# Kernel optimization log

Measured on AMD Instinct MI355X. Metric: run time of the kernel, lower is better.

The kernel has to match this reference:

```python
import jax, jax.numpy as jnp
import numpy as np

NEG_INF = -jnp.inf

def setup_inputs() -> dict:
    key = jax.random.key(0)
    k1, k2, k3, k4, k5 = jax.random.split(key, 5)
    b, n, d = 8, 1024, 2048
    s = 1.0 / np.sqrt(d)  # keep activations well-scaled (kaiming-ish)
    return {
        "y":  jax.random.normal(k1, (b, n, d), dtype=jnp.float32),
        "Wk": jax.random.normal(k2, (d, d), dtype=jnp.float32) * s,
        "Wq": jax.random.normal(k3, (d, d), dtype=jnp.float32) * s,
        "Wv": jax.random.normal(k4, (d, d), dtype=jnp.float32) * s,
        "Wo": jax.random.normal(k5, (d, d), dtype=jnp.float32) * s,
    }

def reference(y, Wk, Wq, Wv, Wo):
    # nn.Linear(bias=False): x @ W.T
    K = jnp.einsum('bnd,ed->bne', y, Wk)
    Q = 0.1 * jnp.einsum('bnd,ed->bne', y, Wq)
    V = jnp.einsum('bnd,ed->bne', y, Wv)
    # logits[b,i,j] = Q_i . K_j
    logits = jnp.einsum('bid,bjd->bij', Q, K)
    n = y.shape[1]
    diag = jnp.eye(n, dtype=bool)  # self-exclusion mask on the diagonal
    logits = jnp.where(diag[None, :, :], NEG_INF, logits)
    # NOTE: softmax over dim=1 (rows of the score matrix), non-standard axis
    attention_weights = jax.nn.softmax(logits, axis=1)
    # dropout(p=0.5) treated as identity (eval/deterministic reference)
    # torch: (V^T @ W)^T  ==  out[b,i,:] = sum_j W[b,j,i] * V[b,j,:]
    out = jnp.einsum('bji,bjd->bid', attention_weights, V)
    out = jnp.einsum('bid,ed->bie', out, Wo)
    return (out, attention_weights)
```

## Files before the change

### kernel.cpp

```cpp
#include <hip/hip_runtime.h>

typedef unsigned short u16;
typedef __attribute__((ext_vector_type(8))) __bf16 bf16x8;
typedef __attribute__((ext_vector_type(4))) float f32x4;
typedef __attribute__((ext_vector_type(4))) unsigned short u16x4;
typedef __attribute__((ext_vector_type(8))) unsigned short u16x8;

#define GLOBAL_AS __attribute__((address_space(1)))
#define LDS_AS __attribute__((address_space(3)))

__device__ __forceinline__ void gload_lds16(const void* g, void* l) {
    __builtin_amdgcn_global_load_lds((const GLOBAL_AS void*)g, (LDS_AS void*)l, 16, 0, 0);
}

__device__ __forceinline__ u16 f2bf(float f) {
    union { float f; unsigned u; } x; x.f = f;
    unsigned r = x.u + 0x7FFFu + ((x.u >> 16) & 1u);
    return (u16)(r >> 16);
}
__device__ __forceinline__ float bf2f(u16 h) {
    union { unsigned u; float f; } x; x.u = ((unsigned)h) << 16;
    return x.f;
}
struct BfPair { u16 h, l; };
__device__ __forceinline__ BfPair split2(float v) {
    BfPair p;
    p.h = f2bf(v);
    p.l = f2bf(v - bf2f(p.h));
    return p;
}

#define TM 128
#define TN 128
#define BK 64

__global__ __launch_bounds__(256) void conv_bf(
    const float* __restrict__ src, u16* __restrict__ dst, int n8)
{
    const int stride = gridDim.x * 256;
    for (int i = blockIdx.x * 256 + threadIdx.x; i < n8; i += stride) {
        const float* g = src + (size_t)i * 8;
        f32x4 v0 = *(const f32x4*)g;
        f32x4 v1 = *(const f32x4*)(g + 4);
        u16x8 w;
        #pragma unroll
        for (int e = 0; e < 4; ++e) { w[e] = f2bf(v0[e]); w[e + 4] = f2bf(v1[e]); }
        *(u16x8*)(dst + (size_t)i * 8) = w;
    }
}

__global__ __launch_bounds__(256) void transpose3(
    const float* __restrict__ s0, const float* __restrict__ s1, const float* __restrict__ s2,
    u16* __restrict__ d0, u16* __restrict__ d1, u16* __restrict__ d2)
{
    __shared__ float tile[64][65];
    const int z = blockIdx.z;
    const float* S = (z == 0) ? s0 : (z == 1) ? s1 : s2;
    u16* D = (z == 0) ? d0 : (z == 1) ? d1 : d2;
    const int x0 = blockIdx.x * 64;
    const int y0 = blockIdx.y * 64;
    const int t = threadIdx.x;
    const int rt = t >> 4;
    const int c4 = (t & 15) * 4;

    #pragma unroll
    for (int p = 0; p < 4; ++p) {
        const int r = p * 16 + rt;
        f32x4 v = *(const f32x4*)(S + (size_t)(y0 + r) * 2048 + x0 + c4);
        #pragma unroll
        for (int e = 0; e < 4; ++e) tile[r][c4 + e] = v[e];
    }
    __syncthreads();
    #pragma unroll
    for (int p = 0; p < 4; ++p) {
        const int a = p * 16 + rt;
        u16x4 w;
        #pragma unroll
        for (int e = 0; e < 4; ++e) w[e] = f2bf(tile[c4 + e][a]);
        *(u16x4*)(D + (size_t)(x0 + a) * 2048 + y0 + c4) = w;
    }
}

__global__ __launch_bounds__(256) void gemm_pre2(
    const u16* __restrict__ A0, const u16* __restrict__ B0,
    u16* __restrict__ GH, u16* __restrict__ GL, float alpha0,
    const u16* __restrict__ A1, const u16* __restrict__ B1, u16* __restrict__ U1,
    int M, int N, int K)
{
    __shared__ u16 As[TM * BK];
    __shared__ u16 Bs[TN * BK];

    const int z = blockIdx.z;
    const u16* Ab = z ? A1 : A0;
    const u16* Bb = z ? B1 : B0;

    const int n0 = blockIdx.x * TN;
    const int m0 = blockIdx.y * TM;
    const int tid = threadIdx.x;
    const int lane = tid & 63;
    const int wave = tid >> 6;
    const int wm = (wave >> 1) * 64;
    const int wn = (wave & 1) * 64;
    const int quad = lane >> 4;
    const int lrow = lane & 15;

    f32x4 acc[4][4] = {};

    for (int k0 = 0; k0 < K; k0 += BK) {
        #pragma unroll
        for (int r = 0; r < 4; ++r) {
            const int wbase = r * 4096 + wave * 1024;
            const int o = wbase + lane * 16;
            const int row = o >> 7;
            const int ce = (o & 127) >> 1;
            gload_lds16(Ab + (size_t)(m0 + row) * K + k0 + ce, (char*)As + wbase);
            gload_lds16(Bb + (size_t)(n0 + row) * K + k0 + ce, (char*)Bs + wbase);
        }
        __syncthreads();

        #pragma unroll
        for (int kk = 0; kk < BK; kk += 32) {
            bf16x8 af[4], bfr[4];
            #pragma unroll
            for (int t = 0; t < 4; ++t) {
                af[t]  = *(const bf16x8*)&As[(wm + t * 16 + lrow) * BK + kk + quad * 8];
                bfr[t] = *(const bf16x8*)&Bs[(wn + t * 16 + lrow) * BK + kk + quad * 8];
            }
            #pragma unroll
            for (int ti = 0; ti < 4; ++ti)
                #pragma unroll
                for (int tj = 0; tj < 4; ++tj)
                    acc[ti][tj] = __builtin_amdgcn_mfma_f32_16x16x32_bf16(
                        af[ti], bfr[tj], acc[ti][tj], 0, 0, 0);
        }
        __syncthreads();
    }

    #pragma unroll
    for (int ti = 0; ti < 4; ++ti)
        #pragma unroll
        for (int tj = 0; tj < 4; ++tj) {
            const int nn = n0 + wn + tj * 16 + lrow;
            #pragma unroll
            for (int r2 = 0; r2 < 4; ++r2) {
                const int mm = m0 + wm + ti * 16 + quad * 4 + r2;
                if (z == 0) {
                    BfPair p = split2(acc[ti][tj][r2] * alpha0);
                    GH[(size_t)mm * N + nn] = p.h;
                    GL[(size_t)mm * N + nn] = p.l;
                } else {
                    U1[(size_t)mm * N + nn] = f2bf(acc[ti][tj][r2]);
                }
            }
        }
}

template <bool OSPLIT>
__global__ __launch_bounds__(256) void gemm_bf(
    const u16* __restrict__ A, const u16* __restrict__ B,
    u16* __restrict__ Ch, u16* __restrict__ Cl,
    int M, int N, int K, size_t sAb, size_t sBb, size_t sCb, float alpha)
{
    __shared__ u16 As[TM * BK];
    __shared__ u16 Bs[TN * BK];

    const int z = blockIdx.z;
    const u16* Ab = (const u16*)((const char*)A + (size_t)z * sAb);
    const u16* Bb = (const u16*)((const char*)B + (size_t)z * sBb);

    const int n0 = blockIdx.x * TN;
    const int m0 = blockIdx.y * TM;
    const int tid = threadIdx.x;
    const int lane = tid & 63;
    const int wave = tid >> 6;
    const int wm = (wave >> 1) * 64;
    const int wn = (wave & 1) * 64;
    const int quad = lane >> 4;
    const int lrow = lane & 15;

    f32x4 acc[4][4] = {};

    for (int k0 = 0; k0 < K; k0 += BK) {
        #pragma unroll
        for (int r = 0; r < 4; ++r) {
            const int wbase = r * 4096 + wave * 1024;
            const int o = wbase + lane * 16;
            const int row = o >> 7;
            const int ce = (o & 127) >> 1;
            gload_lds16(Ab + (size_t)(m0 + row) * K + k0 + ce, (char*)As + wbase);
            gload_lds16(Bb + (size_t)(n0 + row) * K + k0 + ce, (char*)Bs + wbase);
        }
        __syncthreads();

        #pragma unroll
        for (int kk = 0; kk < BK; kk += 32) {
            bf16x8 af[4], bfr[4];
            #pragma unroll
            for (int t = 0; t < 4; ++t) {
                af[t]  = *(const bf16x8*)&As[(wm + t * 16 + lrow) * BK + kk + quad * 8];
                bfr[t] = *(const bf16x8*)&Bs[(wn + t * 16 + lrow) * BK + kk + quad * 8];
            }
            #pragma unroll
            for (int ti = 0; ti < 4; ++ti)
                #pragma unroll
                for (int tj = 0; tj < 4; ++tj)
                    acc[ti][tj] = __builtin_amdgcn_mfma_f32_16x16x32_bf16(
                        af[ti], bfr[tj], acc[ti][tj], 0, 0, 0);
        }
        __syncthreads();
    }

    u16* Chb = (u16*)((char*)Ch + (size_t)z * sCb);
    u16* Clb = OSPLIT ? (u16*)((char*)Cl + (size_t)z * sCb) : nullptr;
    #pragma unroll
    for (int ti = 0; ti < 4; ++ti)
        #pragma unroll
        for (int tj = 0; tj < 4; ++tj) {
            const int nn = n0 + wn + tj * 16 + lrow;
            #pragma unroll
            for (int r2 = 0; r2 < 4; ++r2) {
                const int mm = m0 + wm + ti * 16 + quad * 4 + r2;
                if (OSPLIT) {
                    BfPair p = split2(acc[ti][tj][r2] * alpha);
                    Chb[(size_t)mm * N + nn] = p.h;
                    Clb[(size_t)mm * N + nn] = p.l;
                } else {
                    Chb[(size_t)mm * N + nn] = f2bf(acc[ti][tj][r2] * alpha);
                }
            }
        }
}

template <bool OSPLIT>
__global__ __launch_bounds__(256) void gemm_bs(
    const u16* __restrict__ A,
    const u16* __restrict__ Bh, const u16* __restrict__ Bl,
    void* __restrict__ C, void* __restrict__ C2,
    int M, int N, int K, size_t sAb, size_t sBb, size_t sCb)
{
    __shared__ u16 As[TM * BK];
    __shared__ u16 Bsh[TN * BK];
    __shared__ u16 Bsl[TN * BK];

    const int z = blockIdx.z;
    const u16* Ab  = (const u16*)((const char*)A + (size_t)z * sAb);
    const u16* Bhb = (const u16*)((const char*)Bh + (size_t)z * sBb);
    const u16* Blb = (const u16*)((const char*)Bl + (size_t)z * sBb);

    const int n0 = blockIdx.x * TN;
    const int m0 = blockIdx.y * TM;
    const int tid = threadIdx.x;
    const int lane = tid & 63;
    const int wave = tid >> 6;
    const int wm = (wave >> 1) * 64;
    const int wn = (wave & 1) * 64;
    const int quad = lane >> 4;
    const int lrow = lane & 15;

    f32x4 acc[4][4] = {};

    for (int k0 = 0; k0 < K; k0 += BK) {
        #pragma unroll
        for (int r = 0; r < 4; ++r) {
            const int wbase = r * 4096 + wave * 1024;
            const int o = wbase + lane * 16;
            const int row = o >> 7;
            const int ce = (o & 127) >> 1;
            const size_t ao = (size_t)(m0 + row) * K + k0 + ce;
            const size_t bo = (size_t)(n0 + row) * K + k0 + ce;
            gload_lds16(Ab + ao, (char*)As + wbase);
            gload_lds16(Bhb + bo, (char*)Bsh + wbase);
            gload_lds16(Blb + bo, (char*)Bsl + wbase);
        }
        __syncthreads();

        #pragma unroll
        for (int kk = 0; kk < BK; kk += 32) {
            bf16x8 af[4], bh[4], bl[4];
            #pragma unroll
            for (int t = 0; t < 4; ++t) {
                const int ra = (wm + t * 16 + lrow) * BK + kk + quad * 8;
                const int rb = (wn + t * 16 + lrow) * BK + kk + quad * 8;
                af[t] = *(const bf16x8*)&As[ra];
                bh[t] = *(const bf16x8*)&Bsh[rb];
                bl[t] = *(const bf16x8*)&Bsl[rb];
            }
            #pragma unroll
            for (int ti = 0; ti < 4; ++ti)
                #pragma unroll
                for (int tj = 0; tj < 4; ++tj) {
                    acc[ti][tj] = __builtin_amdgcn_mfma_f32_16x16x32_bf16(
                        af[ti], bl[tj], acc[ti][tj], 0, 0, 0);
                    acc[ti][tj] = __builtin_amdgcn_mfma_f32_16x16x32_bf16(
                        af[ti], bh[tj], acc[ti][tj], 0, 0, 0);
                }
        }
        __syncthreads();
    }

    if (OSPLIT) {
        u16* Chb = (u16*)((char*)C + (size_t)z * sCb);
        u16* Clb = (u16*)((char*)C2 + (size_t)z * sCb);
        #pragma unroll
        for (int ti = 0; ti < 4; ++ti)
            #pragma unroll
            for (int tj = 0; tj < 4; ++tj) {
                const int nn = n0 + wn + tj * 16 + lrow;
                #pragma unroll
                for (int r2 = 0; r2 < 4; ++r2) {
                    const int mm = m0 + wm + ti * 16 + quad * 4 + r2;
                    BfPair p = split2(acc[ti][tj][r2]);
                    Chb[(size_t)mm * N + nn] = p.h;
                    Clb[(size_t)mm * N + nn] = p.l;
                }
            }
    } else {
        float* Cb = (float*)((char*)C + (size_t)z * sCb);
        #pragma unroll
        for (int ti = 0; ti < 4; ++ti)
            #pragma unroll
            for (int tj = 0; tj < 4; ++tj) {
                const int nn = n0 + wn + tj * 16 + lrow;
                #pragma unroll
                for (int r2 = 0; r2 < 4; ++r2) {
                    const int mm = m0 + wm + ti * 16 + quad * 4 + r2;
                    Cb[(size_t)mm * N + nn] = acc[ti][tj][r2];
                }
            }
    }
}

__global__ __launch_bounds__(256) void gemm_fin(
    const u16* __restrict__ Ah, const u16* __restrict__ Al,
    const u16* __restrict__ B, float* __restrict__ C,
    int M, int N, int K, size_t sAb, size_t sBb, size_t sCb)
{
    __shared__ u16 Ash[TM * BK];
    __shared__ u16 Asl[TM * BK];
    __shared__ u16 Bs[TN * BK];

    const int z = blockIdx.z;
    const u16* Ahb = (const u16*)((const char*)Ah + (size_t)z * sAb);
    const u16* Alb = (const u16*)((const char*)Al + (size_t)z * sAb);
    const u16* Bb  = (const u16*)((const char*)B + (size_t)z * sBb);

    const int n0 = blockIdx.x * TN;
    const int m0 = blockIdx.y * TM;
    const int tid = threadIdx.x;
    const int lane = tid & 63;
    const int wave = tid >> 6;
    const int wm = (wave >> 1) * 64;
    const int wn = (wave & 1) * 64;
    const int quad = lane >> 4;
    const int lrow = lane & 15;

    f32x4 acc[4][4] = {};

    for (int k0 = 0; k0 < K; k0 += BK) {
        #pragma unroll
        for (int r = 0; r < 4; ++r) {
            const int wbase = r * 4096 + wave * 1024;
            const int o = wbase + lane * 16;
            const int row = o >> 7;
            const int ce = (o & 127) >> 1;
            const size_t ao = (size_t)(m0 + row) * K + k0 + ce;
            const size_t bo = (size_t)(n0 + row) * K + k0 + ce;
            gload_lds16(Ahb + ao, (char*)Ash + wbase);
            gload_lds16(Alb + ao, (char*)Asl + wbase);
            gload_lds16(Bb + bo, (char*)Bs + wbase);
        }
        __syncthreads();

        #pragma unroll
        for (int kk = 0; kk < BK; kk += 32) {
            bf16x8 ah[4], al[4], bfr[4];
            #pragma unroll
            for (int t = 0; t < 4; ++t) {
                const int ra = (wm + t * 16 + lrow) * BK + kk + quad * 8;
                ah[t] = *(const bf16x8*)&Ash[ra];
                al[t] = *(const bf16x8*)&Asl[ra];
                bfr[t] = *(const bf16x8*)&Bs[(wn + t * 16 + lrow) * BK + kk + quad * 8];
            }
            #pragma unroll
            for (int ti = 0; ti < 4; ++ti)
                #pragma unroll
                for (int tj = 0; tj < 4; ++tj) {
                    acc[ti][tj] = __builtin_amdgcn_mfma_f32_16x16x32_bf16(
                        al[ti], bfr[tj], acc[ti][tj], 0, 0, 0);
                    acc[ti][tj] = __builtin_amdgcn_mfma_f32_16x16x32_bf16(
                        ah[ti], bfr[tj], acc[ti][tj], 0, 0, 0);
                }
        }
        __syncthreads();
    }

    float* Cb = (float*)((char*)C + (size_t)z * sCb);
    #pragma unroll
    for (int ti = 0; ti < 4; ++ti)
        #pragma unroll
        for (int tj = 0; tj < 4; ++tj) {
            const int nn = n0 + wn + tj * 16 + lrow;
            #pragma unroll
            for (int r2 = 0; r2 < 4; ++r2) {
                const int mm = m0 + wm + ti * 16 + quad * 4 + r2;
                Cb[(size_t)mm * N + nn] = acc[ti][tj][r2];
            }
        }
}

__global__ __launch_bounds__(256) void softmax_split(
    const float* __restrict__ Lh, u16* __restrict__ Th, u16* __restrict__ Tl)
{
    const int lane = threadIdx.x & 63;
    const int wave = threadIdx.x >> 6;
    const size_t row = (size_t)blockIdx.x * 4 + wave;
    const int i = (int)(row & 1023);
    const float* src = Lh + row * 1024;
    const float NEG = -__builtin_inff();

    float v[16];
    float mx = NEG;
    #pragma unroll
    for (int cc = 0; cc < 4; ++cc) {
        f32x4 x = *(const f32x4*)(src + cc * 256 + lane * 4);
        #pragma unroll
        for (int e = 0; e < 4; ++e) {
            const int j = cc * 256 + lane * 4 + e;
            const float val = (j == i) ? NEG : x[e];
            v[cc * 4 + e] = val;
            mx = fmaxf(mx, val);
        }
    }
    #pragma unroll
    for (int off = 32; off > 0; off >>= 1) mx = fmaxf(mx, __shfl_xor(mx, off, 64));
    float s = 0.f;
    #pragma unroll
    for (int k = 0; k < 16; ++k) { v[k] = __expf(v[k] - mx); s += v[k]; }
    #pragma unroll
    for (int off = 32; off > 0; off >>= 1) s += __shfl_xor(s, off, 64);
    const float inv = 1.0f / s;

    #pragma unroll
    for (int cc = 0; cc < 4; ++cc) {
        u16x4 wh, wl;
        #pragma unroll
        for (int e = 0; e < 4; ++e) {
            BfPair p = split2(v[cc * 4 + e] * inv);
            wh[e] = p.h;
            wl[e] = p.l;
        }
        *(u16x4*)(Th + row * 1024 + cc * 256 + lane * 4) = wh;
        *(u16x4*)(Tl + row * 1024 + cc * 256 + lane * 4) = wl;
    }
}

__global__ __launch_bounds__(256) void transpose_attn_f32(
    const u16* __restrict__ Th, const u16* __restrict__ Tl, float* __restrict__ A)
{
    __shared__ float tile[64][65];
    const int bz = blockIdx.z;
    const int x0 = blockIdx.x * 64;
    const int y0 = blockIdx.y * 64;
    const size_t base = (size_t)bz * 1024 * 1024;
    float* dst = A + base;
    const int t = threadIdx.x;
    const int rt = t >> 4;
    const int c4 = (t & 15) * 4;

    #pragma unroll
    for (int p = 0; p < 4; ++p) {
        const int r = p * 16 + rt;
        const size_t off = base + (size_t)(y0 + r) * 1024 + x0 + c4;
        u16x4 vh = *(const u16x4*)(Th + off);
        u16x4 vl = *(const u16x4*)(Tl + off);
        #pragma unroll
        for (int e = 0; e < 4; ++e) tile[r][c4 + e] = bf2f(vh[e]) + bf2f(vl[e]);
    }
    __syncthreads();
    #pragma unroll
    for (int p = 0; p < 4; ++p) {
        const int a = p * 16 + rt;
        f32x4 w;
        #pragma unroll
        for (int e = 0; e < 4; ++e) w[e] = tile[c4 + e][a];
        *(f32x4*)(dst + (size_t)(x0 + a) * 1024 + y0 + c4) = w;
    }
}

extern "C" void kernel_launch(void* const* d_in, const int* in_sizes, int n_in,
                              void* d_out, int out_size, void* d_ws, size_t ws_size,
                              hipStream_t stream) {
    const float* y  = (const float*)d_in[0];
    const float* Wk = (const float*)d_in[1];
    const float* Wq = (const float*)d_in[2];
    const float* Wv = (const float*)d_in[3];
    const float* Wo = (const float*)d_in[4];

    const int b = 8, n = 1024, d = 2048;
    const int MB = b * n;
    const size_t MiB = 1024 * 1024;

    char* ws = (char*)d_ws;
    u16* yB  = (u16*)(ws);
    u16* WkT = (u16*)(ws + 32 * MiB);
    u16* WqT = (u16*)(ws + 40 * MiB);
    u16* WvT = (u16*)(ws + 48 * MiB);
    u16* WoB = (u16*)(ws + 56 * MiB);
    u16* GtH = (u16*)(ws + 64 * MiB);
    u16* GtL = (u16*)(ws + 72 * MiB);
    u16* UtB = (u16*)(ws + 80 * MiB);
    u16* ZcH = (u16*)(ws + 32 * MiB);
    u16* ZcL = (u16*)(ws + 88 * MiB);
    u16* Th  = (u16*)(ws + 32 * MiB);
    u16* Tl  = (u16*)(ws + 48 * MiB);
    u16* VOt = (u16*)(ws + 88 * MiB);

    float* outF = (float*)d_out;
    float* attF = outF + (size_t)MB * d;
    float* Lh   = (float*)d_out;

    dim3 blk(256);
    conv_bf<<<dim3(2048), blk, 0, stream>>>(y,  yB,  (MB * d) / 8);
    conv_bf<<<dim3(512),  blk, 0, stream>>>(Wo, WoB, (d * d) / 8);
    transpose3<<<dim3(32, 32, 3), blk, 0, stream>>>(Wk, Wq, Wv, WkT, WqT, WvT);
    gemm_pre2<<<dim3(d / TN, d / TM, 2), blk, 0, stream>>>(
        WkT, WqT, GtH, GtL, 0.1f, WoB, WvT, UtB, d, d, d);
    gemm_bs<true><<<dim3(d / TN, MB / TM, 1), blk, 0, stream>>>(
        yB, GtH, GtL, ZcH, ZcL, MB, d, d, 0, 0, 0);
    gemm_bs<false><<<dim3(n / TN, n / TM, b), blk, 0, stream>>>(
        yB, ZcH, ZcL, Lh, nullptr, n, n, d,
        (size_t)n * d * 2, (size_t)n * d * 2, (size_t)n * n * 4);
    softmax_split<<<dim3(MB / 4), blk, 0, stream>>>(Lh, Th, Tl);
    transpose_attn_f32<<<dim3(16, 16, b), blk, 0, stream>>>(Th, Tl, attF);
    gemm_bf<false><<<dim3(n / TN, d / TM, b), blk, 0, stream>>>(
        UtB, yB, VOt, nullptr, d, n, d, 0, (size_t)n * d * 2, (size_t)d * n * 2, 1.0f);
    gemm_fin<<<dim3(d / TN, n / TM, b), blk, 0, stream>>>(
        Th, Tl, VOt, outF, n, d, n,
        (size_t)n * n * 2, (size_t)d * n * 2, (size_t)n * d * 4);
}
```

Baseline: 656.8 us.

## Replace final two GEMMs with triple-buffered swizzled 256x128 pipelined GEMM kernel

Adds a gemm_dp kernel with 512 threads, a 256x128 output tile, a three-stage LDS ring filled via global_load_lds, and an XOR-swizzled LDS layout. A partial vmcnt wait lets the next tiles load while the current one is being computed. The final hi/lo split product becomes a single GEMM over a concatenated K axis (Th then Tl against VOt twice), replacing the paired MFMAs per step. The aim is to hide memory latency and reduce LDS bank conflicts. The cost is about 147KB of LDS per block, so only one block fits per CU despite the launch bound of two.

Measured after the change: 677.1 us. 3.1% more time.

```diff
diff --git a/kernel.cpp b/kernel.cpp
--- a/kernel.cpp
+++ b/kernel.cpp
@@ -150,82 +150,6 @@
                     GL[(size_t)mm * N + nn] = p.l;
                 } else {
                     U1[(size_t)mm * N + nn] = f2bf(acc[ti][tj][r2]);
-                }
-            }
-        }
-}
-
-template <bool OSPLIT>
-__global__ __launch_bounds__(256) void gemm_bf(
-    const u16* __restrict__ A, const u16* __restrict__ B,
-    u16* __restrict__ Ch, u16* __restrict__ Cl,
-    int M, int N, int K, size_t sAb, size_t sBb, size_t sCb, float alpha)
-{
-    __shared__ u16 As[TM * BK];
-    __shared__ u16 Bs[TN * BK];
-
-    const int z = blockIdx.z;
-    const u16* Ab = (const u16*)((const char*)A + (size_t)z * sAb);
-    const u16* Bb = (const u16*)((const char*)B + (size_t)z * sBb);
-
-    const int n0 = blockIdx.x * TN;
-    const int m0 = blockIdx.y * TM;
-    const int tid = threadIdx.x;
-    const int lane = tid & 63;
-    const int wave = tid >> 6;
-    const int wm = (wave >> 1) * 64;
-    const int wn = (wave & 1) * 64;
-    const int quad = lane >> 4;
-    const int lrow = lane & 15;
-
-    f32x4 acc[4][4] = {};
-
-    for (int k0 = 0; k0 < K; k0 += BK) {
-        #pragma unroll
-        for (int r = 0; r < 4; ++r) {
-            const int wbase = r * 4096 + wave * 1024;
-            const int o = wbase + lane * 16;
-            const int row = o >> 7;
-            const int ce = (o & 127) >> 1;
-            gload_lds16(Ab + (size_t)(m0 + row) * K + k0 + ce, (char*)As + wbase);
-            gload_lds16(Bb + (size_t)(n0 + row) * K + k0 + ce, (char*)Bs + wbase);
-        }
-        __syncthreads();
-
-        #pragma unroll
-        for (int kk = 0; kk < BK; kk += 32) {
-            bf16x8 af[4], bfr[4];
-            #pragma unroll
-            for (int t = 0; t < 4; ++t) {
-                af[t]  = *(const bf16x8*)&As[(wm + t * 16 + lrow) * BK + kk + quad * 8];
-                bfr[t] = *(const bf16x8*)&Bs[(wn + t * 16 + lrow) * BK + kk + quad * 8];
-            }
-            #pragma unroll
-            for (int ti = 0; ti < 4; ++ti)
-                #pragma unroll
-                for (int tj = 0; tj < 4; ++tj)
-                    acc[ti][tj] = __builtin_amdgcn_mfma_f32_16x16x32_bf16(
-                        af[ti], bfr[tj], acc[ti][tj], 0, 0, 0);
-        }
-        __syncthreads();
-    }
-
-    u16* Chb = (u16*)((char*)Ch + (size_t)z * sCb);
-    u16* Clb = OSPLIT ? (u16*)((char*)Cl + (size_t)z * sCb) : nullptr;
-    #pragma unroll
-    for (int ti = 0; ti < 4; ++ti)
-        #pragma unroll
-        for (int tj = 0; tj < 4; ++tj) {
-            const int nn = n0 + wn + tj * 16 + lrow;
-            #pragma unroll
-            for (int r2 = 0; r2 < 4; ++r2) {
-                const int mm = m0 + wm + ti * 16 + quad * 4 + r2;
-                if (OSPLIT) {
-                    BfPair p = split2(acc[ti][tj][r2] * alpha);
-                    Chb[(size_t)mm * N + nn] = p.h;
-                    Clb[(size_t)mm * N + nn] = p.l;
-                } else {
-                    Chb[(size_t)mm * N + nn] = f2bf(acc[ti][tj][r2] * alpha);
                 }
             }
         }
@@ -330,80 +254,120 @@
     }
 }
 
-__global__ __launch_bounds__(256) void gemm_fin(
-    const u16* __restrict__ Ah, const u16* __restrict__ Al,
-    const u16* __restrict__ B, float* __restrict__ C,
-    int M, int N, int K, size_t sAb, size_t sBb, size_t sCb)
-{
-    __shared__ u16 Ash[TM * BK];
-    __shared__ u16 Asl[TM * BK];
-    __shared__ u16 Bs[TN * BK];
+#define DBM 256
+#define DBN 128
+template <int EPI>
+__global__ __launch_bounds__(512, 2) void gemm_dp(
+    const u16* __restrict__ A0, const u16* __restrict__ A1, int halfKA, int ldA, size_t sAb,
+    const u16* __restrict__ B0, const u16* __restrict__ B1, int halfKB, int ldB, size_t sBb,
+    void* __restrict__ C, size_t sCb, int M, int N, int Ktot)
+{
+    __shared__ alignas(16) u16 As[3 * DBM * BK];
+    __shared__ alignas(16) u16 Bs[3 * DBN * BK];
 
     const int z = blockIdx.z;
-    const u16* Ahb = (const u16*)((const char*)Ah + (size_t)z * sAb);
-    const u16* Alb = (const u16*)((const char*)Al + (size_t)z * sAb);
-    const u16* Bb  = (const u16*)((const char*)B + (size_t)z * sBb);
-
-    const int n0 = blockIdx.x * TN;
-    const int m0 = blockIdx.y * TM;
+    const u16* A0b = (const u16*)((const char*)A0 + (size_t)z * sAb);
+    const u16* A1b = (const u16*)((const char*)A1 + (size_t)z * sAb);
+    const u16* B0b = (const u16*)((const char*)B0 + (size_t)z * sBb);
+    const u16* B1b = (const u16*)((const char*)B1 + (size_t)z * sBb);
+
+    const int n0 = blockIdx.x * DBN;
+    const int m0 = blockIdx.y * DBM;
     const int tid = threadIdx.x;
     const int lane = tid & 63;
-    const int wave = tid >> 6;
-    const int wm = (wave >> 1) * 64;
-    const int wn = (wave & 1) * 64;
+    const int wid = tid >> 6;
+    const int wr = wid >> 1;
+    const int wc = wid & 1;
     const int quad = lane >> 4;
     const int lrow = lane & 15;
 
+    int arow[4], acol[4], brow[2], bcol[2];
+    #pragma unroll
+    for (int s = 0; s < 4; ++s) {
+        const int o = s * 8192 + tid * 16;
+        const int L = o ^ (((o >> 9) & 1) << 5);
+        arow[s] = L >> 7; acol[s] = L & 127;
+    }
+    #pragma unroll
+    for (int s = 0; s < 2; ++s) {
+        const int o = s * 8192 + tid * 16;
+        const int L = o ^ (((o >> 9) & 1) << 5);
+        brow[s] = L >> 7; bcol[s] = L & 127;
+    }
+    const int ldst = wid * 1024;
+
+    const int NT = Ktot / BK;
+
+    auto STAGE = [&](int tt, int bufi) {
+        const int k0 = tt * BK;
+        const u16* Ap = (k0 < halfKA) ? A0b : A1b;
+        const int ka = (k0 < halfKA) ? k0 : k0 - halfKA;
+        const u16* Bp = (k0 < halfKB) ? B0b : B1b;
+        const int kb = (k0 < halfKB) ? k0 : k0 - halfKB;
+        char* ab = (char*)As + bufi * (DBM * BK * 2);
+        char* bb = (char*)Bs + bufi * (DBN * BK * 2);
+        #pragma unroll
+        for (int s = 0; s < 4; ++s)
+            gload_lds16((const char*)Ap + ((size_t)(m0 + arow[s]) * ldA + ka) * 2 + acol[s],
+                        ab + s * 8192 + ldst);
+        #pragma unroll
+        for (int s = 0; s < 2; ++s)
+            gload_lds16((const char*)Bp + ((size_t)(n0 + brow[s]) * ldB + kb) * 2 + bcol[s],
+                        bb + s * 8192 + ldst);
+    };
+
     f32x4 acc[4][4] = {};
 
-    for (int k0 = 0; k0 < K; k0 += BK) {
-        #pragma unroll
-        for (int r = 0; r < 4; ++r) {
-            const int wbase = r * 4096 + wave * 1024;
-            const int o = wbase + lane * 16;
-            const int row = o >> 7;
-            const int ce = (o & 127) >> 1;
-            const size_t ao = (size_t)(m0 + row) * K + k0 + ce;
-            const size_t bo = (size_t)(n0 + row) * K + k0 + ce;
-            gload_lds16(Ahb + ao, (char*)Ash + wbase);
-            gload_lds16(Alb + ao, (char*)Asl + wbase);
-            gload_lds16(Bb + bo, (char*)Bs + wbase);
-        }
-        __syncthreads();
-
+    STAGE(0, 0); STAGE(1, 1); STAGE(2, 2);
+
+    int cur = 0;
+    for (int t = 0; t < NT; ++t) {
+        asm volatile("s_waitcnt vmcnt(12)" ::: "memory");
+        __builtin_amdgcn_s_barrier();
+        __builtin_amdgcn_sched_barrier(0);
+
+        const char* ab = (const char*)As + cur * (DBM * BK * 2);
+        const char* bb = (const char*)Bs + cur * (DBN * BK * 2);
         #pragma unroll
         for (int kk = 0; kk < BK; kk += 32) {
-            bf16x8 ah[4], al[4], bfr[4];
-            #pragma unroll
-            for (int t = 0; t < 4; ++t) {
-                const int ra = (wm + t * 16 + lrow) * BK + kk + quad * 8;
-                ah[t] = *(const bf16x8*)&Ash[ra];
-                al[t] = *(const bf16x8*)&Asl[ra];
-                bfr[t] = *(const bf16x8*)&Bs[(wn + t * 16 + lrow) * BK + kk + quad * 8];
+            bf16x8 af[4], bfr[4];
+            const int cbase = kk * 2 + quad * 16;
+            #pragma unroll
+            for (int f = 0; f < 4; ++f) {
+                const int ra = wr * 64 + f * 16 + lrow;
+                af[f] = *(const bf16x8*)(ab + ra * 128 + (cbase ^ (((ra >> 2) & 1) << 5)));
+                const int rb = wc * 64 + f * 16 + lrow;
+                bfr[f] = *(const bf16x8*)(bb + rb * 128 + (cbase ^ (((rb >> 2) & 1) << 5)));
             }
             #pragma unroll
             for (int ti = 0; ti < 4; ++ti)
                 #pragma unroll
-                for (int tj = 0; tj < 4; ++tj) {
+                for (int tj = 0; tj < 4; ++tj)
                     acc[ti][tj] = __builtin_amdgcn_mfma_f32_16x16x32_bf16(
-                        al[ti], bfr[tj], acc[ti][tj], 0, 0, 0);
-                    acc[ti][tj] = __builtin_amdgcn_mfma_f32_16x16x32_bf16(
-                        ah[ti], bfr[tj], acc[ti][tj], 0, 0, 0);
+                        af[ti], bfr[tj], acc[ti][tj], 0, 0, 0);
+        }
+        __builtin_amdgcn_sched_barrier(0);
+        __builtin_amdgcn_s_barrier();
+        __builtin_amdgcn_sched_barrier(0);
+        if (t + 3 < NT) STAGE(t + 3, cur);
+        cur = (cur == 2) ? 0 : cur + 1;
+    }
+
+    #pragma unroll
+    for (int ti = 0; ti < 4; ++ti)
+        #pragma unroll
+        for (int tj = 0; tj < 4; ++tj) {
+            const int nn = n0 + wc * 64 + tj * 16 + lrow;
+            #pragma unroll
+            for (int r2 = 0; r2 < 4; ++r2) {
+                const int mm = m0 + wr * 64 + ti * 16 + quad * 4 + r2;
+                if (EPI == 0) {
+                    float* Cb = (float*)((char*)C + (size_t)z * sCb);
+                    Cb[(size_t)mm * N + nn] = acc[ti][tj][r2];
+                } else {
+                    u16* Cb = (u16*)((char*)C + (size_t)z * sCb);
+                    Cb[(size_t)mm * N + nn] = f2bf(acc[ti][tj][r2]);
                 }
-        }
-        __syncthreads();
-    }
-
-    float* Cb = (float*)((char*)C + (size_t)z * sCb);
-    #pragma unroll
-    for (int ti = 0; ti < 4; ++ti)
-        #pragma unroll
-        for (int tj = 0; tj < 4; ++tj) {
-            const int nn = n0 + wn + tj * 16 + lrow;
-            #pragma unroll
-            for (int r2 = 0; r2 < 4; ++r2) {
-                const int mm = m0 + wm + ti * 16 + quad * 4 + r2;
-                Cb[(size_t)mm * N + nn] = acc[ti][tj][r2];
             }
         }
 }
@@ -520,6 +484,7 @@
     float* Lh   = (float*)d_out;
 
     dim3 blk(256);
+    dim3 blk5(512);
     conv_bf<<<dim3(2048), blk, 0, stream>>>(y,  yB,  (MB * d) / 8);
     conv_bf<<<dim3(512),  blk, 0, stream>>>(Wo, WoB, (d * d) / 8);
     transpose3<<<dim3(32, 32, 3), blk, 0, stream>>>(Wk, Wq, Wv, WkT, WqT, WvT);
@@ -532,9 +497,12 @@
         (size_t)n * d * 2, (size_t)n * d * 2, (size_t)n * n * 4);
     softmax_split<<<dim3(MB / 4), blk, 0, stream>>>(Lh, Th, Tl);
     transpose_attn_f32<<<dim3(16, 16, b), blk, 0, stream>>>(Th, Tl, attF);
-    gemm_bf<false><<<dim3(n / TN, d / TM, b), blk, 0, stream>>>(
-        UtB, yB, VOt, nullptr, d, n, d, 0, (size_t)n * d * 2, (size_t)d * n * 2, 1.0f);
-    gemm_fin<<<dim3(d / TN, n / TM, b), blk, 0, stream>>>(
-        Th, Tl, VOt, outF, n, d, n,
-        (size_t)n * n * 2, (size_t)d * n * 2, (size_t)n * d * 4);
-}
+    gemm_dp<2><<<dim3(n / DBN, d / DBM, b), blk5, 0, stream>>>(
+        UtB, UtB, d, d, 0,
+        yB, yB, d, d, (size_t)n * d * 2,
+        VOt, (size_t)d * n * 2, d, n, d);
+    gemm_dp<0><<<dim3(d / DBN, n / DBM, b), blk5, 0, stream>>>(
+        Th, Tl, n, n, (size_t)n * n * 2,
+        VOt, VOt, n, n, (size_t)d * n * 2,
+        outF, (size_t)n * d * 4, n, d, 2 * n);
+}
```
